# Kernel optimization log

Measured on AMD Instinct MI355X. Metric: run time of the kernel, lower is better.

Reference implementation:

```python
import jax, jax.numpy as jnp
import numpy as np

N, K, D, VOCAB = 20000, 32, 128, 100000
NEG = -1e30  # finite large-negative so all-masked rows don't produce NaN softmax


def setup_inputs() -> dict:
    key = jax.random.key(0)
    ks = jax.random.split(key, 10)
    return {
        "nodes": jax.random.randint(ks[0], (N,), 0, VOCAB),
        "neigh_idx": jax.random.randint(ks[1], (N, K), 0, VOCAB),
        "neigh_len": jax.random.randint(ks[2], (N,), 0, K + 1),
        "u2e": jax.random.normal(ks[3], (VOCAB, D), dtype=jnp.float32),
        "W1": jax.random.normal(ks[4], (D, 2 * D), dtype=jnp.float32) * 0.05,
        "b1": jax.random.normal(ks[5], (D,), dtype=jnp.float32) * 0.05,
        "W2": jax.random.normal(ks[6], (D, D), dtype=jnp.float32) * 0.05,
        "b2": jax.random.normal(ks[7], (D,), dtype=jnp.float32) * 0.05,
        "W3": jax.random.normal(ks[8], (1, D), dtype=jnp.float32) * 0.05,
        "b3": jax.random.normal(ks[9], (1,), dtype=jnp.float32) * 0.05,
    }


def reference(nodes, neigh_idx, neigh_len, u2e, W1, b1, W2, b2, W3, b3):
    # self features: [N, D]
    self_feats = u2e[nodes]
    # neighbor features gather: [N, K, D]
    e_u = u2e[neigh_idx]
    # GraphRec Attention: cat(neighbor, self-broadcast) -> MLP -> softmax over K
    x = jnp.concatenate(
        [e_u, jnp.broadcast_to(self_feats[:, None, :], e_u.shape)], axis=-1
    )  # [N, K, 2D]
    h = jax.nn.relu(jnp.einsum("nkf,df->nkd", x, W1) + b1)
    h = jax.nn.relu(jnp.einsum("nkd,ed->nke", h, W2) + b2)
    logits = jnp.einsum("nkd,od->nko", h, W3)[..., 0] + b3[0]  # [N, K]
    mask = jnp.arange(K)[None, :] < neigh_len[:, None]  # [N, K]
    att = jax.nn.softmax(jnp.where(mask, logits, NEG), axis=1)
    att = jnp.where(mask, att, 0.0)  # zero out padded slots (and all-empty rows)
    # attention-weighted neighbor aggregation: [N, D]
    agg = jnp.einsum("nk,nkd->nd", att, e_u)
    has_neigh = (neigh_len > 0)[:, None]
    return jnp.where(has_neigh, (agg + self_feats) * 0.5, self_feats)
```

## Files before the change

kernel.cpp:

```cpp
#include <hip/hip_runtime.h>
#include <hip/hip_bf16.h>
#include <stdint.h>

#define KN 32
#define D  128
#define NNODES 20000
#define GRID 2500
#define ITERS 4
#define VOCAB 100000
#define SV1_BLOCKS ((NNODES + 127) / 128)

typedef __bf16 bf16;
typedef __bf16 bf16x8 __attribute__((ext_vector_type(8)));
typedef float  f32x4  __attribute__((ext_vector_type(4)));

#define CHUNK_E 520
#define EU_NODE_E (8 * CHUNK_E)
#define H_STRIDE 136

#define GL2LDS(src, dst) __builtin_amdgcn_global_load_lds(                 \
    (const __attribute__((address_space(1))) void*)(src),                  \
    (__attribute__((address_space(3))) void*)(dst), 16, 0, 0)

#define MFMA(a, b, c) __builtin_amdgcn_mfma_f32_16x16x32_bf16((a), (b), (c), 0, 0, 0)

__global__ __launch_bounds__(256) void pack_weights_kernel(
    const float* __restrict__ W1, const float* __restrict__ W2,
    bf16* __restrict__ w1p, bf16* __restrict__ w2p)
{
    int t = blockIdx.x * 256 + threadIdx.x;
    if (t < 32768) {
        int j = t & 7, lane = (t >> 3) & 63, kt = (t >> 9) & 7, nt = t >> 12;
        int d = nt * 16 + (lane & 15);
        int f = kt * 32 + ((lane >> 4) << 3) + j;
        w1p[t] = (bf16)W1[d * 256 + f];
    } else if (t < 49152) {
        int u = t - 32768;
        int j = u & 7, lane = (u >> 3) & 63, kt = (u >> 9) & 3, nt = u >> 11;
        int e  = nt * 16 + (lane & 15);
        int dd = kt * 32 + ((lane >> 4) << 3) + j;
        w2p[u] = (bf16)W2[e * 128 + dd];
    }
}

__global__ __launch_bounds__(256) void convert_table_kernel(
    const float* __restrict__ u2e, bf16* __restrict__ tbl)
{
    size_t i = ((size_t)blockIdx.x * 256 + threadIdx.x) * 8;
    float4 a = *(const float4*)(u2e + i);
    float4 b = *(const float4*)(u2e + i + 4);
    bf16x8 v;
    v[0]=(bf16)a.x; v[1]=(bf16)a.y; v[2]=(bf16)a.z; v[3]=(bf16)a.w;
    v[4]=(bf16)b.x; v[5]=(bf16)b.y; v[6]=(bf16)b.z; v[7]=(bf16)b.w;
    *(bf16x8*)(tbl + i) = v;
}

__global__ __launch_bounds__(256) void sv1_kernel(
    const int*  __restrict__ nodes,
    const bf16* __restrict__ u2e_bf,
    const bf16* __restrict__ w1p,
    float*      __restrict__ sv1t)
{
    __shared__ alignas(16) bf16 sr[4 * EU_NODE_E];

    const int t    = threadIdx.x;
    const int lane = t & 63;
    const int wave = t >> 6;
    const int ln15 = lane & 15;
    const int quad = lane >> 4;
    const int r0   = blockIdx.x * 128;

    #pragma unroll
    for (int c = 0; c < 8; ++c) {
        int grow = r0 + wave * 32 + c + ((lane >> 4) << 3);
        int node = nodes[grow < NNODES ? grow : NNODES - 1];
        GL2LDS(u2e_bf + (size_t)node * D + ((lane & 15) << 3),
               sr + wave * EU_NODE_E + c * CHUNK_E);
    }
    __syncthreads();

    const bf16* g  = sr + wave * EU_NODE_E;
    const int   rb = (ln15 & 7) * CHUNK_E + (ln15 >> 3) * 128;

    #pragma unroll 1
    for (int np = 0; np < 4; ++np) {
        int nt0 = np * 2;
        bf16x8 b0[4], b1[4];
        #pragma unroll
        for (int kt = 0; kt < 4; ++kt) {
            b0[kt] = *(const bf16x8*)(w1p + (nt0 * 8 + 4 + kt) * 512 + lane * 8);
            b1[kt] = *(const bf16x8*)(w1p + ((nt0 + 1) * 8 + 4 + kt) * 512 + lane * 8);
        }
        f32x4 c00 = {0.f,0.f,0.f,0.f}, c01 = c00, c10 = c00, c11 = c00;
        #pragma unroll
        for (int kt = 0; kt < 4; ++kt) {
            bf16x8 a0 = *(const bf16x8*)(g + rb + kt * 32 + quad * 8);
            bf16x8 a1 = *(const bf16x8*)(g + rb + 256 + kt * 32 + quad * 8);
            c00 = MFMA(a0, b0[kt], c00);
            c01 = MFMA(a0, b1[kt], c01);
            c10 = MFMA(a1, b0[kt], c10);
            c11 = MFMA(a1, b1[kt], c11);
        }
        #pragma unroll
        for (int r = 0; r < 4; ++r) {
            int row = quad * 4 + r;
            int gr0 = r0 + wave * 32 + row;
            int gr1 = gr0 + 16;
            if (gr0 < NNODES) {
                sv1t[(size_t)gr0 * D + nt0 * 16 + ln15]       = c00[r];
                sv1t[(size_t)gr0 * D + (nt0 + 1) * 16 + ln15] = c01[r];
            }
            if (gr1 < NNODES) {
                sv1t[(size_t)gr1 * D + nt0 * 16 + ln15]       = c10[r];
                sv1t[(size_t)gr1 * D + (nt0 + 1) * 16 + ln15] = c11[r];
            }
        }
    }
}

__global__ __launch_bounds__(256, 4) void graphrec_agg_kernel(
    const int*   __restrict__ nodes,
    const int*   __restrict__ neigh_idx,
    const int*   __restrict__ neigh_len,
    const float* __restrict__ u2e,
    const bf16*  __restrict__ u2e_bf,
    const float* __restrict__ sv1t,
    const float* __restrict__ b1,
    const float* __restrict__ b2,
    const float* __restrict__ W3,
    const float* __restrict__ b3,
    const bf16*  __restrict__ w1p,
    const bf16*  __restrict__ w2p,
    float*       __restrict__ out)
{
    __shared__ alignas(16) bf16  eu[2 * EU_NODE_E];
    __shared__ alignas(16) float self_f[2 * D];
    __shared__ alignas(16) bf16  h1[2 * KN * H_STRIDE];
    __shared__ float lpart[2][4 * KN];

    const int t    = threadIdx.x;
    const int lane = t & 63;
    const int wave = t >> 6;
    const int ln15 = lane & 15;
    const int quad = lane >> 4;
    const int nt0  = wave * 2;

    const float bias1_0 = b1[nt0 * 16 + ln15];
    const float bias1_1 = b1[(nt0 + 1) * 16 + ln15];
    const float bias2_0 = b2[nt0 * 16 + ln15];
    const float bias2_1 = b2[(nt0 + 1) * 16 + ln15];
    const float w3_0    = W3[nt0 * 16 + ln15];
    const float w3_1    = W3[(nt0 + 1) * 16 + ln15];
    const float b3v     = b3[0];

    bf16x8 w1r[2][4];
    #pragma unroll
    for (int nt = 0; nt < 2; ++nt)
        #pragma unroll
        for (int ft = 0; ft < 4; ++ft)
            w1r[nt][ft] = *(const bf16x8*)(w1p + ((nt0 + nt) * 8 + ft) * 512 + lane * 8);
    bf16x8 w2r[2][4];
    #pragma unroll
    for (int nt = 0; nt < 2; ++nt)
        #pragma unroll
        for (int kt = 0; kt < 4; ++kt)
            w2r[nt][kt] = *(const bf16x8*)(w2p + ((nt0 + nt) * 4 + kt) * 512 + lane * 8);

    #pragma unroll 1
    for (int it = 0; it < ITERS; ++it) {
        const int nA   = blockIdx.x * 8 + it * 2;
        const int lenA = neigh_len[nA];
        const int lenB = neigh_len[nA + 1];

        const float svA0 = sv1t[(size_t)nA * D + nt0 * 16 + ln15];
        const float svA1 = sv1t[(size_t)nA * D + (nt0 + 1) * 16 + ln15];
        const float svB0 = sv1t[(size_t)(nA + 1) * D + nt0 * 16 + ln15];
        const float svB1 = sv1t[(size_t)(nA + 1) * D + (nt0 + 1) * 16 + ln15];

        {
            const int gnd = wave >> 1;
            const int cb  = (wave & 1) * 4;
            #pragma unroll
            for (int j = 0; j < 4; ++j) {
                int chunk = cb + j;
                int idx = neigh_idx[(nA + gnd) * KN + chunk + ((lane >> 4) << 3)];
                GL2LDS(u2e_bf + (size_t)idx * D + ((lane & 15) << 3),
                       eu + gnd * EU_NODE_E + chunk * CHUNK_E);
            }
            if (wave == 0) {
                int sidx = nodes[nA + (lane >> 5)];
                GL2LDS(u2e + (size_t)sidx * D + ((lane & 31) << 2), self_f);
            }
        }
        __syncthreads();

        #pragma unroll 1
        for (int nd = 0; nd < 2; ++nd) {
            const bf16* euN = eu + nd * EU_NODE_E;
            bf16* h1N = h1 + nd * KN * H_STRIDE;

            f32x4 c00 = {0.f,0.f,0.f,0.f}, c01 = c00, c10 = c00, c11 = c00;
            const int rb = (ln15 & 7) * CHUNK_E + (ln15 >> 3) * 128;
            #pragma unroll
            for (int ft = 0; ft < 4; ++ft) {
                bf16x8 a0 = *(const bf16x8*)(euN + rb + ft * 32 + quad * 8);
                bf16x8 a1 = *(const bf16x8*)(euN + rb + 256 + ft * 32 + quad * 8);
                c00 = MFMA(a0, w1r[0][ft], c00);
                c01 = MFMA(a0, w1r[1][ft], c01);
                c10 = MFMA(a1, w1r[0][ft], c10);
                c11 = MFMA(a1, w1r[1][ft], c11);
            }
            const float s0 = nd ? svB0 : svA0;
            const float s1 = nd ? svB1 : svA1;
            #pragma unroll
            for (int r = 0; r < 4; ++r) {
                int row = quad * 4 + r;
                h1N[row * H_STRIDE + nt0 * 16 + ln15]              = (bf16)fmaxf(c00[r] + bias1_0 + s0, 0.f);
                h1N[row * H_STRIDE + (nt0 + 1) * 16 + ln15]        = (bf16)fmaxf(c01[r] + bias1_1 + s1, 0.f);
                h1N[(16 + row) * H_STRIDE + nt0 * 16 + ln15]       = (bf16)fmaxf(c10[r] + bias1_0 + s0, 0.f);
                h1N[(16 + row) * H_STRIDE + (nt0 + 1) * 16 + ln15] = (bf16)fmaxf(c11[r] + bias1_1 + s1, 0.f);
            }
        }
        __syncthreads();

        #pragma unroll 1
        for (int nd = 0; nd < 2; ++nd) {
            const bf16* h1N = h1 + nd * KN * H_STRIDE;
            f32x4 d00 = {0.f,0.f,0.f,0.f}, d01 = d00, d10 = d00, d11 = d00;
            #pragma unroll
            for (int kt = 0; kt < 4; ++kt) {
                bf16x8 a0 = *(const bf16x8*)(h1N + ln15 * H_STRIDE + kt * 32 + quad * 8);
                bf16x8 a1 = *(const bf16x8*)(h1N + (16 + ln15) * H_STRIDE + kt * 32 + quad * 8);
                d00 = MFMA(a0, w2r[0][kt], d00);
                d01 = MFMA(a0, w2r[1][kt], d01);
                d10 = MFMA(a1, w2r[0][kt], d10);
                d11 = MFMA(a1, w2r[1][kt], d11);
            }
            #pragma unroll
            for (int r = 0; r < 4; ++r) {
                float p0 = w3_0 * fmaxf(d00[r] + bias2_0, 0.f)
                         + w3_1 * fmaxf(d01[r] + bias2_1, 0.f);
                float p1 = w3_0 * fmaxf(d10[r] + bias2_0, 0.f)
                         + w3_1 * fmaxf(d11[r] + bias2_1, 0.f);
                #pragma unroll
                for (int o = 1; o < 16; o <<= 1) {
                    p0 += __shfl_xor(p0, o);
                    p1 += __shfl_xor(p1, o);
                }
                if (ln15 == 0) {
                    lpart[nd][wave * KN + quad * 4 + r]      = p0;
                    lpart[nd][wave * KN + 16 + quad * 4 + r] = p1;
                }
            }
        }
        __syncthreads();

        {
            const int nd = wave >> 1;
            const int k  = lane & 31;
            float lg = lpart[nd][k] + lpart[nd][KN + k] + lpart[nd][2 * KN + k]
                     + lpart[nd][3 * KN + k] + b3v;
            const int len = nd ? lenB : lenA;
            bool act = k < len;
            float l = act ? lg : -1e30f;
            float m = l;
            #pragma unroll
            for (int o = 1; o < 32; o <<= 1) m = fmaxf(m, __shfl_xor(m, o));
            float e = act ? expf(l - m) : 0.f;
            float s = e;
            #pragma unroll
            for (int o = 1; o < 32; o <<= 1) s += __shfl_xor(s, o);
            float att = (s > 0.f) ? (e / s) : 0.f;

            const int d = ((wave & 1) << 6) + lane;
            const bf16* euN = eu + nd * EU_NODE_E;
            float acc = 0.f;
            #pragma unroll
            for (int k2 = 0; k2 < KN; ++k2) {
                float a  = __shfl(att, k2);
                float ev = (float)euN[(k2 & 7) * CHUNK_E + (k2 >> 3) * 128 + (d & 127)];
                acc += a * ev;
            }
            float sf = self_f[nd * D + (d & 127)];
            out[(size_t)(nA + nd) * D + (d & 127)] = (len > 0) ? 0.5f * (acc + sf) : sf;
        }
        __syncthreads();
    }
}

#define FB_CHUNK_DW 260
#define FB_EU_NODE_DW (16 * FB_CHUNK_DW)

__global__ __launch_bounds__(256, 3) void graphrec_agg_fb(
    const int*   __restrict__ nodes,
    const int*   __restrict__ neigh_idx,
    const int*   __restrict__ neigh_len,
    const float* __restrict__ u2e,
    const float* __restrict__ b1,
    const float* __restrict__ b2,
    const float* __restrict__ W3,
    const float* __restrict__ b3,
    const bf16*  __restrict__ w1p,
    const bf16*  __restrict__ w2p,
    float*       __restrict__ out)
{
    __shared__ alignas(16) float eu[2 * FB_EU_NODE_DW];
    __shared__ alignas(16) bf16  h1[2 * KN * H_STRIDE];
    __shared__ alignas(16) float self_f[2 * D];
    __shared__ float lpart[2][4 * KN];
    __shared__ float att_s[2][KN];

    const int t    = threadIdx.x;
    const int lane = t & 63;
    const int wave = t >> 6;
    const int ln15 = lane & 15;
    const int quad = lane >> 4;
    const int nt0  = wave * 2;

    const float bias1_0 = b1[nt0 * 16 + ln15];
    const float bias1_1 = b1[(nt0 + 1) * 16 + ln15];
    const float bias2_0 = b2[nt0 * 16 + ln15];
    const float bias2_1 = b2[(nt0 + 1) * 16 + ln15];
    const float w3_0    = W3[nt0 * 16 + ln15];
    const float w3_1    = W3[(nt0 + 1) * 16 + ln15];
    const float b3v     = b3[0];

    bf16x8 w1r[2][8];
    #pragma unroll
    for (int nt = 0; nt < 2; ++nt)
        #pragma unroll
        for (int ft = 0; ft < 8; ++ft)
            w1r[nt][ft] = *(const bf16x8*)(w1p + ((nt0 + nt) * 8 + ft) * 512 + lane * 8);
    bf16x8 w2r[2][4];
    #pragma unroll
    for (int nt = 0; nt < 2; ++nt)
        #pragma unroll
        for (int kt = 0; kt < 4; ++kt)
            w2r[nt][kt] = *(const bf16x8*)(w2p + ((nt0 + nt) * 4 + kt) * 512 + lane * 8);

    #pragma unroll 1
    for (int it = 0; it < ITERS; ++it) {
        const int nA   = blockIdx.x * 8 + it * 2;
        const int lenA = neigh_len[nA];
        const int lenB = neigh_len[nA + 1];
        {
            const int half = lane >> 5;
            const int colb = (lane & 31) << 4;
            #pragma unroll
            for (int nd = 0; nd < 2; ++nd) {
                #pragma unroll
                for (int j = 0; j < 4; ++j) {
                    int chunk = wave * 4 + j;
                    int idx = neigh_idx[(nA + nd) * KN + chunk + (half << 4)];
                    const char* src = (const char*)(u2e + (size_t)idx * D) + colb;
                    GL2LDS(src, eu + nd * FB_EU_NODE_DW + chunk * FB_CHUNK_DW);
                }
            }
            if (wave == 0) {
                int sidx = nodes[nA + half];
                const char* src = (const char*)(u2e + (size_t)sidx * D) + colb;
                GL2LDS(src, self_f);
            }
        }
        __syncthreads();
        #pragma unroll 1
        for (int nd = 0; nd < 2; ++nd) {
            const float* euN = eu + nd * FB_EU_NODE_DW;
            const float* sfN = self_f + nd * D;
            bf16* h1N = h1 + nd * KN * H_STRIDE;
            f32x4 c00 = {0.f,0.f,0.f,0.f}, c01 = c00, c10 = c00, c11 = c00;
            const int r0 = ln15 * FB_CHUNK_DW;
            #pragma unroll
            for (int ft = 0; ft < 4; ++ft) {
                int off = ft * 32 + quad * 8;
                f32x4 u0 = *(const f32x4*)(euN + r0 + off);
                f32x4 u1 = *(const f32x4*)(euN + r0 + off + 4);
                f32x4 v0 = *(const f32x4*)(euN + r0 + 128 + off);
                f32x4 v1 = *(const f32x4*)(euN + r0 + 128 + off + 4);
                bf16x8 a0, a1;
                #pragma unroll
                for (int e = 0; e < 4; ++e) {
                    a0[e] = (bf16)u0[e]; a0[4 + e] = (bf16)u1[e];
                    a1[e] = (bf16)v0[e]; a1[4 + e] = (bf16)v1[e];
                }
                c00 = MFMA(a0, w1r[0][ft], c00);
                c01 = MFMA(a0, w1r[1][ft], c01);
                c10 = MFMA(a1, w1r[0][ft], c10);
                c11 = MFMA(a1, w1r[1][ft], c11);
            }
            #pragma unroll
            for (int ft = 4; ft < 8; ++ft) {
                int off = (ft - 4) * 32 + quad * 8;
                f32x4 u0 = *(const f32x4*)(sfN + off);
                f32x4 u1 = *(const f32x4*)(sfN + off + 4);
                bf16x8 a;
                #pragma unroll
                for (int e = 0; e < 4; ++e) { a[e] = (bf16)u0[e]; a[4 + e] = (bf16)u1[e]; }
                c00 = MFMA(a, w1r[0][ft], c00);
                c01 = MFMA(a, w1r[1][ft], c01);
                c10 = MFMA(a, w1r[0][ft], c10);
                c11 = MFMA(a, w1r[1][ft], c11);
            }
            #pragma unroll
            for (int r = 0; r < 4; ++r) {
                int row = quad * 4 + r;
                h1N[row * H_STRIDE + nt0 * 16 + ln15]              = (bf16)fmaxf(c00[r] + bias1_0, 0.f);
                h1N[row * H_STRIDE + (nt0 + 1) * 16 + ln15]        = (bf16)fmaxf(c01[r] + bias1_1, 0.f);
                h1N[(16 + row) * H_STRIDE + nt0 * 16 + ln15]       = (bf16)fmaxf(c10[r] + bias1_0, 0.f);
                h1N[(16 + row) * H_STRIDE + (nt0 + 1) * 16 + ln15] = (bf16)fmaxf(c11[r] + bias1_1, 0.f);
            }
        }
        __syncthreads();
        #pragma unroll 1
        for (int nd = 0; nd < 2; ++nd) {
            const bf16* h1N = h1 + nd * KN * H_STRIDE;
            f32x4 d00 = {0.f,0.f,0.f,0.f}, d01 = d00, d10 = d00, d11 = d00;
            #pragma unroll
            for (int kt = 0; kt < 4; ++kt) {
                bf16x8 a0 = *(const bf16x8*)(h1N + ln15 * H_STRIDE + kt * 32 + quad * 8);
                bf16x8 a1 = *(const bf16x8*)(h1N + (16 + ln15) * H_STRIDE + kt * 32 + quad * 8);
                d00 = MFMA(a0, w2r[0][kt], d00);
                d01 = MFMA(a0, w2r[1][kt], d01);
                d10 = MFMA(a1, w2r[0][kt], d10);
                d11 = MFMA(a1, w2r[1][kt], d11);
            }
            #pragma unroll
            for (int r = 0; r < 4; ++r) {
                float p0 = w3_0 * fmaxf(d00[r] + bias2_0, 0.f)
                         + w3_1 * fmaxf(d01[r] + bias2_1, 0.f);
                float p1 = w3_0 * fmaxf(d10[r] + bias2_0, 0.f)
                         + w3_1 * fmaxf(d11[r] + bias2_1, 0.f);
                #pragma unroll
                for (int o = 1; o < 16; o <<= 1) {
                    p0 += __shfl_xor(p0, o);
                    p1 += __shfl_xor(p1, o);
                }
                if (ln15 == 0) {
                    lpart[nd][wave * KN + quad * 4 + r]      = p0;
                    lpart[nd][wave * KN + 16 + quad * 4 + r] = p1;
                }
            }
        }
        __syncthreads();
        if (wave < 2) {
            int nd = wave, k = lane & 31;
            float lg = lpart[nd][k] + lpart[nd][KN + k] + lpart[nd][2 * KN + k]
                     + lpart[nd][3 * KN + k] + b3v;
            int len = nd ? lenB : lenA;
            bool act = (lane < 32) && (k < len);
            float l = act ? lg : -1e30f;
            float m = l;
            #pragma unroll
            for (int o = 1; o < 32; o <<= 1) m = fmaxf(m, __shfl_xor(m, o));
            float e = act ? expf(l - m) : 0.f;
            float s = e;
            #pragma unroll
            for (int o = 1; o < 32; o <<= 1) s += __shfl_xor(s, o);
            if (lane < 32) att_s[nd][k] = (s > 0.f) ? (e / s) : 0.f;
        }
        __syncthreads();
        {
            int nd = t >> 7, d = t & 127;
            const float* euN = eu + nd * FB_EU_NODE_DW;
            float acc = 0.f;
            #pragma unroll
            for (int k = 0; k < KN; ++k)
                acc += att_s[nd][k] * euN[(k & 15) * FB_CHUNK_DW + ((k >> 4) << 7) + d];
            float sf = self_f[nd * D + d];
            int len = nd ? lenB : lenA;
            out[(size_t)(nA + nd) * D + d] = (len > 0) ? 0.5f * (acc + sf) : sf;
        }
        __syncthreads();
    }
}

extern "C" void kernel_launch(void* const* d_in, const int* in_sizes, int n_in,
                              void* d_out, int out_size, void* d_ws, size_t ws_size,
                              hipStream_t stream) {
    const int*   nodes     = (const int*)d_in[0];
    const int*   neigh_idx = (const int*)d_in[1];
    const int*   neigh_len = (const int*)d_in[2];
    const float* u2e       = (const float*)d_in[3];
    const float* W1        = (const float*)d_in[4];
    const float* b1        = (const float*)d_in[5];
    const float* W2        = (const float*)d_in[6];
    const float* b2        = (const float*)d_in[7];
    const float* W3        = (const float*)d_in[8];
    const float* b3        = (const float*)d_in[9];
    float* out = (float*)d_out;

    bf16*  w1p    = (bf16*)d_ws;
    bf16*  w2p    = w1p + 32768;
    bf16*  u2e_bf = (bf16*)((char*)d_ws + 98304);
    float* sv1t   = (float*)((char*)d_ws + 98304 + (size_t)VOCAB * D * 2);
    const size_t need = 98304ull + (size_t)VOCAB * D * 2 + (size_t)NNODES * D * 4;

    pack_weights_kernel<<<192, 256, 0, stream>>>(W1, W2, w1p, w2p);
    if (ws_size >= need) {
        convert_table_kernel<<<VOCAB * D / 2048, 256, 0, stream>>>(u2e, u2e_bf);
        sv1_kernel<<<SV1_BLOCKS, 256, 0, stream>>>(nodes, u2e_bf, w1p, sv1t);
        graphrec_agg_kernel<<<GRID, 256, 0, stream>>>(nodes, neigh_idx, neigh_len,
                                                      u2e, u2e_bf, sv1t, b1, b2,
                                                      W3, b3, w1p, w2p, out);
    } else {
        graphrec_agg_fb<<<GRID, 256, 0, stream>>>(nodes, neigh_idx, neigh_len, u2e,
                                                  b1, b2, W3, b3, w1p, w2p, out);
    }
}
```

Baseline: 217.5 us.

## Fuse prep kernels, compute self projection in-kernel, double-buffer neighbor gathers

Merges table conversion and weight packing into one prep kernel and drops the separate self-feature projection kernel along with its intermediate buffer. The main kernel now computes the self half of the first layer itself with MFMA, using the fp32 self features cast to bf16. Neighbor and self gathers are double-buffered in LDS, so the next iteration's loads are issued before the current compute and waited on with partial vmcnt counts. This saves two launches and a global round trip, but uses more LDS and registers, and occupancy is lowered to 3 blocks.

New measurement: 212.9 us. 1.02x faster.

```diff
diff --git a/kernel.cpp b/kernel.cpp
--- a/kernel.cpp
+++ b/kernel.cpp
@@ -8,7 +8,7 @@
 #define GRID 2500
 #define ITERS 4
 #define VOCAB 100000
-#define SV1_BLOCKS ((NNODES + 127) / 128)
+#define CONV_BLOCKS (VOCAB * D / 2048)
 
 typedef __bf16 bf16;
 typedef __bf16 bf16x8 __attribute__((ext_vector_type(8)));
@@ -23,6 +23,13 @@
     (__attribute__((address_space(3))) void*)(dst), 16, 0, 0)
 
 #define MFMA(a, b, c) __builtin_amdgcn_mfma_f32_16x16x32_bf16((a), (b), (c), 0, 0, 0)
+
+#define LBAR() do {                                                        \
+    asm volatile("s_waitcnt lgkmcnt(0)" ::: "memory");                     \
+    __builtin_amdgcn_s_barrier();                                          \
+    asm volatile("" ::: "memory");                                         \
+    __builtin_amdgcn_sched_barrier(0);                                     \
+} while (0)
 
 __global__ __launch_bounds__(256) void pack_weights_kernel(
     const float* __restrict__ W1, const float* __restrict__ W2,
@@ -43,88 +50,43 @@
     }
 }
 
-__global__ __launch_bounds__(256) void convert_table_kernel(
-    const float* __restrict__ u2e, bf16* __restrict__ tbl)
+__global__ __launch_bounds__(256) void prep_kernel(
+    const float* __restrict__ u2e, const float* __restrict__ W1,
+    const float* __restrict__ W2,
+    bf16* __restrict__ tbl, bf16* __restrict__ w1p, bf16* __restrict__ w2p)
 {
-    size_t i = ((size_t)blockIdx.x * 256 + threadIdx.x) * 8;
-    float4 a = *(const float4*)(u2e + i);
-    float4 b = *(const float4*)(u2e + i + 4);
-    bf16x8 v;
-    v[0]=(bf16)a.x; v[1]=(bf16)a.y; v[2]=(bf16)a.z; v[3]=(bf16)a.w;
-    v[4]=(bf16)b.x; v[5]=(bf16)b.y; v[6]=(bf16)b.z; v[7]=(bf16)b.w;
-    *(bf16x8*)(tbl + i) = v;
-}
-
-__global__ __launch_bounds__(256) void sv1_kernel(
-    const int*  __restrict__ nodes,
-    const bf16* __restrict__ u2e_bf,
-    const bf16* __restrict__ w1p,
-    float*      __restrict__ sv1t)
-{
-    __shared__ alignas(16) bf16 sr[4 * EU_NODE_E];
-
-    const int t    = threadIdx.x;
-    const int lane = t & 63;
-    const int wave = t >> 6;
-    const int ln15 = lane & 15;
-    const int quad = lane >> 4;
-    const int r0   = blockIdx.x * 128;
-
-    #pragma unroll
-    for (int c = 0; c < 8; ++c) {
-        int grow = r0 + wave * 32 + c + ((lane >> 4) << 3);
-        int node = nodes[grow < NNODES ? grow : NNODES - 1];
-        GL2LDS(u2e_bf + (size_t)node * D + ((lane & 15) << 3),
-               sr + wave * EU_NODE_E + c * CHUNK_E);
-    }
-    __syncthreads();
-
-    const bf16* g  = sr + wave * EU_NODE_E;
-    const int   rb = (ln15 & 7) * CHUNK_E + (ln15 >> 3) * 128;
-
-    #pragma unroll 1
-    for (int np = 0; np < 4; ++np) {
-        int nt0 = np * 2;
-        bf16x8 b0[4], b1[4];
-        #pragma unroll
-        for (int kt = 0; kt < 4; ++kt) {
-            b0[kt] = *(const bf16x8*)(w1p + (nt0 * 8 + 4 + kt) * 512 + lane * 8);
-            b1[kt] = *(const bf16x8*)(w1p + ((nt0 + 1) * 8 + 4 + kt) * 512 + lane * 8);
-        }
-        f32x4 c00 = {0.f,0.f,0.f,0.f}, c01 = c00, c10 = c00, c11 = c00;
-        #pragma unroll
-        for (int kt = 0; kt < 4; ++kt) {
-            bf16x8 a0 = *(const bf16x8*)(g + rb + kt * 32 + quad * 8);
-            bf16x8 a1 = *(const bf16x8*)(g + rb + 256 + kt * 32 + quad * 8);
-            c00 = MFMA(a0, b0[kt], c00);
-            c01 = MFMA(a0, b1[kt], c01);
-            c10 = MFMA(a1, b0[kt], c10);
-            c11 = MFMA(a1, b1[kt], c11);
-        }
-        #pragma unroll
-        for (int r = 0; r < 4; ++r) {
-            int row = quad * 4 + r;
-            int gr0 = r0 + wave * 32 + row;
-            int gr1 = gr0 + 16;
-            if (gr0 < NNODES) {
-                sv1t[(size_t)gr0 * D + nt0 * 16 + ln15]       = c00[r];
-                sv1t[(size_t)gr0 * D + (nt0 + 1) * 16 + ln15] = c01[r];
-            }
-            if (gr1 < NNODES) {
-                sv1t[(size_t)gr1 * D + nt0 * 16 + ln15]       = c10[r];
-                sv1t[(size_t)gr1 * D + (nt0 + 1) * 16 + ln15] = c11[r];
-            }
+    int b = blockIdx.x;
+    if (b < CONV_BLOCKS) {
+        size_t i = ((size_t)b * 256 + threadIdx.x) * 8;
+        float4 a = *(const float4*)(u2e + i);
+        float4 c = *(const float4*)(u2e + i + 4);
+        bf16x8 v;
+        v[0]=(bf16)a.x; v[1]=(bf16)a.y; v[2]=(bf16)a.z; v[3]=(bf16)a.w;
+        v[4]=(bf16)c.x; v[5]=(bf16)c.y; v[6]=(bf16)c.z; v[7]=(bf16)c.w;
+        *(bf16x8*)(tbl + i) = v;
+    } else {
+        int t = (b - CONV_BLOCKS) * 256 + threadIdx.x;
+        if (t < 32768) {
+            int j = t & 7, lane = (t >> 3) & 63, kt = (t >> 9) & 7, nt = t >> 12;
+            int d = nt * 16 + (lane & 15);
+            int f = kt * 32 + ((lane >> 4) << 3) + j;
+            w1p[t] = (bf16)W1[d * 256 + f];
+        } else if (t < 49152) {
+            int u = t - 32768;
+            int j = u & 7, lane = (u >> 3) & 63, kt = (u >> 9) & 3, nt = u >> 11;
+            int e  = nt * 16 + (lane & 15);
+            int dd = kt * 32 + ((lane >> 4) << 3) + j;
+            w2p[u] = (bf16)W2[e * 128 + dd];
         }
     }
 }
 
-__global__ __launch_bounds__(256, 4) void graphrec_agg_kernel(
+__global__ __launch_bounds__(256, 3) void graphrec_agg_kernel(
     const int*   __restrict__ nodes,
     const int*   __restrict__ neigh_idx,
     const int*   __restrict__ neigh_len,
     const float* __restrict__ u2e,
     const bf16*  __restrict__ u2e_bf,
-    const float* __restrict__ sv1t,
     const float* __restrict__ b1,
     const float* __restrict__ b2,
     const float* __restrict__ W3,
@@ -133,8 +95,8 @@
     const bf16*  __restrict__ w2p,
     float*       __restrict__ out)
 {
-    __shared__ alignas(16) bf16  eu[2 * EU_NODE_E];
-    __shared__ alignas(16) float self_f[2 * D];
+    __shared__ alignas(16) bf16  eu[2][2 * EU_NODE_E];
+    __shared__ alignas(16) float self_f[2][2 * D];
     __shared__ alignas(16) bf16  h1[2 * KN * H_STRIDE];
     __shared__ float lpart[2][4 * KN];
 
@@ -153,18 +115,40 @@
     const float w3_1    = W3[(nt0 + 1) * 16 + ln15];
     const float b3v     = b3[0];
 
-    bf16x8 w1r[2][4];
+    bf16x8 w1e[2][4], w1s[2][4], w2r[2][4];
     #pragma unroll
-    for (int nt = 0; nt < 2; ++nt)
+    for (int nt = 0; nt < 2; ++nt) {
         #pragma unroll
-        for (int ft = 0; ft < 4; ++ft)
-            w1r[nt][ft] = *(const bf16x8*)(w1p + ((nt0 + nt) * 8 + ft) * 512 + lane * 8);
-    bf16x8 w2r[2][4];
-    #pragma unroll
-    for (int nt = 0; nt < 2; ++nt)
+        for (int ft = 0; ft < 4; ++ft) {
+            w1e[nt][ft] = *(const bf16x8*)(w1p + ((nt0 + nt) * 8 + ft) * 512 + lane * 8);
+            w1s[nt][ft] = *(const bf16x8*)(w1p + ((nt0 + nt) * 8 + 4 + ft) * 512 + lane * 8);
+        }
         #pragma unroll
         for (int kt = 0; kt < 4; ++kt)
             w2r[nt][kt] = *(const bf16x8*)(w2p + ((nt0 + nt) * 4 + kt) * 512 + lane * 8);
+    }
+
+    auto STAGE = [&](int jt) {
+        const int buf = jt & 1;
+        const int nA2 = blockIdx.x * 8 + jt * 2;
+        const int gnd = wave >> 1;
+        const int cb  = (wave & 1) * 4;
+        const int sA  = nodes[nA2];
+        const int sB  = nodes[nA2 + 1];
+        int4 idx4 = *(const int4*)(neigh_idx + (size_t)(nA2 + gnd) * KN + cb + (quad << 3));
+        bf16* dst = &eu[buf][gnd * EU_NODE_E + cb * CHUNK_E];
+        const size_t col = (size_t)(ln15 << 3);
+        GL2LDS(u2e_bf + (size_t)idx4.x * D + col, dst);
+        GL2LDS(u2e_bf + (size_t)idx4.y * D + col, dst + CHUNK_E);
+        GL2LDS(u2e_bf + (size_t)idx4.z * D + col, dst + 2 * CHUNK_E);
+        GL2LDS(u2e_bf + (size_t)idx4.w * D + col, dst + 3 * CHUNK_E);
+        if (wave == 0) {
+            int sidx = (lane >> 5) ? sB : sA;
+            GL2LDS(u2e + (size_t)sidx * D + ((lane & 31) << 2), &self_f[buf][0]);
+        }
+    };
+
+    STAGE(0);
 
     #pragma unroll 1
     for (int it = 0; it < ITERS; ++it) {
@@ -172,31 +156,44 @@
         const int lenA = neigh_len[nA];
         const int lenB = neigh_len[nA + 1];
 
-        const float svA0 = sv1t[(size_t)nA * D + nt0 * 16 + ln15];
-        const float svA1 = sv1t[(size_t)nA * D + (nt0 + 1) * 16 + ln15];
-        const float svB0 = sv1t[(size_t)(nA + 1) * D + nt0 * 16 + ln15];
-        const float svB1 = sv1t[(size_t)(nA + 1) * D + (nt0 + 1) * 16 + ln15];
-
+        if (it + 1 < ITERS) STAGE(it + 1);
+        __builtin_amdgcn_sched_barrier(0);
+        if (it == 0 || it + 1 == ITERS) {
+            asm volatile("s_waitcnt vmcnt(0)" ::: "memory");
+        } else if (wave == 0) {
+            asm volatile("s_waitcnt vmcnt(6)" ::: "memory");
+        } else {
+            asm volatile("s_waitcnt vmcnt(5)" ::: "memory");
+        }
+        __builtin_amdgcn_s_barrier();
+        asm volatile("" ::: "memory");
+        __builtin_amdgcn_sched_barrier(0);
+
+        const bf16*  euIt = &eu[it & 1][0];
+        const float* sfIt = &self_f[it & 1][0];
+
+        f32x4 cs0 = {0.f,0.f,0.f,0.f}, cs1 = cs0;
         {
-            const int gnd = wave >> 1;
-            const int cb  = (wave & 1) * 4;
-            #pragma unroll
-            for (int j = 0; j < 4; ++j) {
-                int chunk = cb + j;
-                int idx = neigh_idx[(nA + gnd) * KN + chunk + ((lane >> 4) << 3)];
-                GL2LDS(u2e_bf + (size_t)idx * D + ((lane & 15) << 3),
-                       eu + gnd * EU_NODE_E + chunk * CHUNK_E);
-            }
-            if (wave == 0) {
-                int sidx = nodes[nA + (lane >> 5)];
-                GL2LDS(u2e + (size_t)sidx * D + ((lane & 31) << 2), self_f);
-            }
-        }
-        __syncthreads();
+            const float* sp = sfIt + (ln15 < 2 ? ln15 : 1) * D;
+            #pragma unroll
+            for (int kt = 0; kt < 4; ++kt) {
+                f32x4 u0 = *(const f32x4*)(sp + kt * 32 + quad * 8);
+                f32x4 u1 = *(const f32x4*)(sp + kt * 32 + quad * 8 + 4);
+                bf16x8 a;
+                #pragma unroll
+                for (int e = 0; e < 4; ++e) { a[e] = (bf16)u0[e]; a[4 + e] = (bf16)u1[e]; }
+                cs0 = MFMA(a, w1s[0][kt], cs0);
+                cs1 = MFMA(a, w1s[1][kt], cs1);
+            }
+        }
+        const float svA0 = __shfl(cs0[0], ln15);
+        const float svB0 = __shfl(cs0[1], ln15);
+        const float svA1 = __shfl(cs1[0], ln15);
+        const float svB1 = __shfl(cs1[1], ln15);
 
         #pragma unroll 1
         for (int nd = 0; nd < 2; ++nd) {
-            const bf16* euN = eu + nd * EU_NODE_E;
+            const bf16* euN = euIt + nd * EU_NODE_E;
             bf16* h1N = h1 + nd * KN * H_STRIDE;
 
             f32x4 c00 = {0.f,0.f,0.f,0.f}, c01 = c00, c10 = c00, c11 = c00;
@@ -205,10 +202,10 @@
             for (int ft = 0; ft < 4; ++ft) {
                 bf16x8 a0 = *(const bf16x8*)(euN + rb + ft * 32 + quad * 8);
                 bf16x8 a1 = *(const bf16x8*)(euN + rb + 256 + ft * 32 + quad * 8);
-                c00 = MFMA(a0, w1r[0][ft], c00);
-                c01 = MFMA(a0, w1r[1][ft], c01);
-                c10 = MFMA(a1, w1r[0][ft], c10);
-                c11 = MFMA(a1, w1r[1][ft], c11);
+                c00 = MFMA(a0, w1e[0][ft], c00);
+                c01 = MFMA(a0, w1e[1][ft], c01);
+                c10 = MFMA(a1, w1e[0][ft], c10);
+                c11 = MFMA(a1, w1e[1][ft], c11);
             }
             const float s0 = nd ? svB0 : svA0;
             const float s1 = nd ? svB1 : svA1;
@@ -221,7 +218,7 @@
                 h1N[(16 + row) * H_STRIDE + (nt0 + 1) * 16 + ln15] = (bf16)fmaxf(c11[r] + bias1_1 + s1, 0.f);
             }
         }
-        __syncthreads();
+        LBAR();
 
         #pragma unroll 1
         for (int nd = 0; nd < 2; ++nd) {
@@ -253,7 +250,7 @@
                 }
             }
         }
-        __syncthreads();
+        LBAR();
 
         {
             const int nd = wave >> 1;
@@ -273,7 +270,7 @@
             float att = (s > 0.f) ? (e / s) : 0.f;
 
             const int d = ((wave & 1) << 6) + lane;
-            const bf16* euN = eu + nd * EU_NODE_E;
+            const bf16* euN = euIt + nd * EU_NODE_E;
             float acc = 0.f;
             #pragma unroll
             for (int k2 = 0; k2 < KN; ++k2) {
@@ -281,10 +278,10 @@
                 float ev = (float)euN[(k2 & 7) * CHUNK_E + (k2 >> 3) * 128 + (d & 127)];
                 acc += a * ev;
             }
-            float sf = self_f[nd * D + (d & 127)];
+            float sf = sfIt[nd * D + (d & 127)];
             out[(size_t)(nA + nd) * D + (d & 127)] = (len > 0) ? 0.5f * (acc + sf) : sf;
         }
-        __syncthreads();
+        LBAR();
     }
 }
 
@@ -492,17 +489,16 @@
     bf16*  w1p    = (bf16*)d_ws;
     bf16*  w2p    = w1p + 32768;
     bf16*  u2e_bf = (bf16*)((char*)d_ws + 98304);
-    float* sv1t   = (float*)((char*)d_ws + 98304 + (size_t)VOCAB * D * 2);
-    const size_t need = 98304ull + (size_t)VOCAB * D * 2 + (size_t)NNODES * D * 4;
-
-    pack_weights_kernel<<<192, 256, 0, stream>>>(W1, W2, w1p, w2p);
+    const size_t need = 98304ull + (size_t)VOCAB * D * 2;
+
     if (ws_size >= need) {
-        convert_table_kernel<<<VOCAB * D / 2048, 256, 0, stream>>>(u2e, u2e_bf);
-        sv1_kernel<<<SV1_BLOCKS, 256, 0, stream>>>(nodes, u2e_bf, w1p, sv1t);
+        prep_kernel<<<CONV_BLOCKS + 192, 256, 0, stream>>>(u2e, W1, W2,
+                                                           u2e_bf, w1p, w2p);
         graphrec_agg_kernel<<<GRID, 256, 0, stream>>>(nodes, neigh_idx, neigh_len,
-                                                      u2e, u2e_bf, sv1t, b1, b2,
+                                                      u2e, u2e_bf, b1, b2,
                                                       W3, b3, w1p, w2p, out);
     } else {
+        pack_weights_kernel<<<192, 256, 0, stream>>>(W1, W2, w1p, w2p);
         graphrec_agg_fb<<<GRID, 256, 0, stream>>>(nodes, neigh_idx, neigh_len, u2e,
                                                   b1, b2, W3, b3, w1p, w2p, out);
     }
```
